# Kernel optimization log

Measured on AMD Instinct MI355X. Metric: run time of the kernel, lower is better.

Reference implementation:

```python
import jax, jax.numpy as jnp
import numpy as np

B, N, C, NH, AG, HW = 16, 3136, 256, 8, 49, 56

def setup_inputs() -> dict:
    key = jax.random.key(0)
    ks = jax.random.split(key, 14)
    f = lambda k, shp, s=0.02: jax.random.normal(k, shp, jnp.float32) * s
    return {
        "x_f": jax.random.normal(ks[0], (B, N, C), jnp.float32),
        "x_t": jax.random.normal(ks[1], (B, N, C), jnp.float32),
        "Wq": f(ks[2], (C, C)),
        "Wkv": f(ks[3], (C, 2 * C)),
        "Wproj": f(ks[4], (C, C)),
        "bproj": jnp.zeros((C,), jnp.float32),
        "dwc_w": f(ks[5], (C, 1, 3, 3), 0.1),   # depthwise 3x3, groups=C (OIHW, I=1)
        "dwc_b": jnp.zeros((C,), jnp.float32),
        "an_bias": f(ks[6], (NH, AG, 7, 7)),
        "na_bias": f(ks[7], (NH, AG, 7, 7)),
        "ah_bias": f(ks[8], (1, NH, AG, HW, 1)),
        "aw_bias": f(ks[9], (1, NH, AG, 1, HW)),
        "ha_bias": f(ks[10], (1, NH, HW, 1, AG)),
        "wa_bias": f(ks[11], (1, NH, 1, HW, AG)),
        "H": HW,
        "W": HW,
    }

def reference(x_f, x_t, Wq, Wkv, Wproj, bproj, dwc_w, dwc_b,
              an_bias, na_bias, ah_bias, aw_bias, ha_bias, wa_bias, H, W):
    b, n, c = x_f.shape
    h, ag = an_bias.shape[0], an_bias.shape[1]
    d = c // h
    scale = d ** (-0.5)
    ps = int(ag ** 0.5)  # agent grid side (7)

    q = x_f @ Wq                       # [b,n,c]
    kv = x_t @ Wkv                     # [b,n,2c]
    k, v = kv[..., :c], kv[..., c:]

    # agent tokens: adaptive avg-pool q over (H,W) -> (ps,ps); H%ps==0 so exact 8x8 block means
    agent = q.reshape(b, ps, H // ps, ps, W // ps, c).mean(axis=(2, 4)).reshape(b, ag, c)

    heads = lambda t, L: t.reshape(b, L, h, d).transpose(0, 2, 1, 3)
    qh, kh, vh, ah = heads(q, n), heads(k, n), heads(v, n), heads(agent, ag)

    # stage 1: agent <- kv attention, bias = bilinear(an_bias 7x7 -> HxW) + (ah + aw)
    pb1 = jax.image.resize(an_bias, (h, ag, H, W), method='bilinear').reshape(1, h, ag, n)
    pb2 = (ah_bias + aw_bias).reshape(1, h, ag, n)
    agent_attn = jax.nn.softmax(scale * jnp.einsum('bhad,bhnd->bhan', ah, kh) + pb1 + pb2, axis=-1)
    agent_v = jnp.einsum('bhan,bhnd->bhad', agent_attn, vh)  # [b,h,ag,d]

    # stage 2: query <- agent attention, bias = bilinear(na_bias)^T + (ha + wa)
    ab1 = jax.image.resize(na_bias, (h, ag, H, W), method='bilinear').reshape(1, h, ag, n).transpose(0, 1, 3, 2)
    ab2 = (ha_bias + wa_bias).reshape(1, h, n, ag)
    q_attn = jax.nn.softmax(scale * jnp.einsum('bhnd,bhad->bhna', qh, ah) + ab1 + ab2, axis=-1)
    x = jnp.einsum('bhna,bhad->bhnd', q_attn, agent_v).transpose(0, 2, 1, 3).reshape(b, n, c)

    # depthwise-conv residual on v
    v_img = vh.transpose(0, 2, 1, 3).reshape(b, H, W, c).transpose(0, 3, 1, 2)  # [b,c,H,W]
    dwc = jax.lax.conv_general_dilated(v_img, dwc_w, (1, 1), 'SAME',
                                       feature_group_count=c,
                                       dimension_numbers=('NCHW', 'OIHW', 'NCHW'))
    dwc = dwc + dwc_b[None, :, None, None]
    x = x + dwc.transpose(0, 2, 3, 1).reshape(b, n, c)

    return x @ Wproj + bproj
```

## Files before the change

### kernel.cpp

```cpp
#include <hip/hip_runtime.h>
#include <hip/hip_bf16.h>

namespace {
constexpr int kB  = 16;
constexpr int kN  = 3136;
constexpr int kC  = 256;
constexpr int kH  = 8;
constexpr int kD  = 32;
constexpr int kAG = 49;
constexpr int kHW = 56;
constexpr int kKV = 512;
constexpr int kSEG = 7;
constexpr int kPART = 33;

constexpr int BM = 128, BN = 128, BK = 64;
constexpr int LDK = BK + 8;

constexpr int kNT = kN / 256 + 1;
}

typedef __attribute__((ext_vector_type(8))) short short8;
typedef __attribute__((ext_vector_type(8))) unsigned short ushort8;
typedef __attribute__((ext_vector_type(4))) unsigned short ushort4v;
typedef __attribute__((ext_vector_type(4))) float f32x4;

__device__ __forceinline__ unsigned short f2bf(float f) {
  union { float f; unsigned u; } v; v.f = f;
  unsigned r = (v.u + 0x7FFF + ((v.u >> 16) & 1)) >> 16;
  return (unsigned short)r;
}
__device__ __forceinline__ float bf2f(unsigned short u) {
  union { unsigned u; float f; } v; v.u = ((unsigned)u) << 16;
  return v.f;
}

__device__ __forceinline__ float bilin7(const float* __restrict__ tab, int y, int x) {
  float fy = (y + 0.5f) * 0.125f - 0.5f;
  float fx = (x + 0.5f) * 0.125f - 0.5f;
  float fy0 = floorf(fy), fx0 = floorf(fx);
  float wy = fy - fy0, wx = fx - fx0;
  int y0 = (int)fy0, x0 = (int)fx0;
  int y0c = min(6, max(0, y0)),     x0c = min(6, max(0, x0));
  int y1c = min(6, max(0, y0 + 1)), x1c = min(6, max(0, x0 + 1));
  float v00 = tab[y0c * 7 + x0c], v01 = tab[y0c * 7 + x1c];
  float v10 = tab[y1c * 7 + x0c], v11 = tab[y1c * 7 + x1c];
  float top = v00 + wx * (v01 - v00);
  float bot = v10 + wx * (v11 - v10);
  return top + wy * (bot - top);
}

__global__ __launch_bounds__(256) void wtrans_kernel(
    const float* __restrict__ W, unsigned short* __restrict__ Wt, int K, int N) {
  int idx = blockIdx.x * 256 + threadIdx.x;
  if (idx >= K * N) return;
  int n = idx / K, k = idx - n * K;
  Wt[idx] = f2bf(W[(size_t)k * N + n]);
}

template <int AMODE, int OMODE>
__global__ __launch_bounds__(256) void gemm_mixed_kernel(
    const void* __restrict__ Ap, const unsigned short* __restrict__ Bt,
    const float* __restrict__ bias, void* __restrict__ Cp, void* __restrict__ Cp2,
    int M, int Nn, int K) {
  __shared__ unsigned short As[BM * LDK];
  __shared__ unsigned short Bs[BN * LDK];
  const int t = threadIdx.x;

  int tx = blockIdx.x, ty = blockIdx.y;
  {
    int nwg = gridDim.x * gridDim.y;
    if ((nwg & 7) == 0) {
      int bid = ty * gridDim.x + tx;
      int per8 = nwg >> 3;
      int lt = (bid & 7) * per8 + (bid >> 3);
      tx = lt % gridDim.x;
      ty = lt / gridDim.x;
    }
  }
  const int row0 = ty * BM;
  const int col0 = tx * BN;
  const int lane = t & 63;
  const int wid  = t >> 6;
  const int wrow = (wid >> 1) * 64;
  const int wcol = (wid & 1) * 64;
  const int lr = lane & 15, lg = lane >> 4;

  f32x4 acc[4][4] = {};

  for (int k0 = 0; k0 < K; k0 += BK) {
    __syncthreads();
    if constexpr (AMODE == 1) {
      const unsigned short* A = (const unsigned short*)Ap;
#pragma unroll
      for (int i = 0; i < 4; ++i) {
        int idx = t + i * 256;
        int r = idx >> 3, k8 = (idx & 7) * 8;
        int row = row0 + r;
        int bb = row / kN, nn = row - bb * kN;
        int k = k0 + k8;
        *(ushort8*)&As[r * LDK + k8] = *(const ushort8*)&A[
            (((size_t)bb * kH + (k >> 5)) * kN + nn) * kD + (k & 31)];
      }
    } else {
      const float* A = (const float*)Ap;
#pragma unroll
      for (int i = 0; i < 8; ++i) {
        int idx = t + i * 256;
        int r = idx >> 4, k4 = (idx & 15) * 4;
        float4 f = *(const float4*)&A[(size_t)(row0 + r) * K + k0 + k4];
        unsigned lo = (unsigned)f2bf(f.x) | ((unsigned)f2bf(f.y) << 16);
        unsigned hi = (unsigned)f2bf(f.z) | ((unsigned)f2bf(f.w) << 16);
        *(uint2*)&As[r * LDK + k4] = make_uint2(lo, hi);
      }
    }
#pragma unroll
    for (int i = 0; i < 4; ++i) {
      int idx = t + i * 256;
      int r = idx >> 3, k8 = (idx & 7) * 8;
      *(ushort8*)&Bs[r * LDK + k8] =
          *(const ushort8*)&Bt[(size_t)(col0 + r) * K + k0 + k8];
    }
    __syncthreads();
#pragma unroll
    for (int ks = 0; ks < 2; ++ks) {
      short8 af[4], bf[4];
#pragma unroll
      for (int m = 0; m < 4; ++m)
        af[m] = *(const short8*)&As[(wrow + m * 16 + lr) * LDK + ks * 32 + lg * 8];
#pragma unroll
      for (int n = 0; n < 4; ++n)
        bf[n] = *(const short8*)&Bs[(wcol + n * 16 + lr) * LDK + ks * 32 + lg * 8];
#pragma unroll
      for (int m = 0; m < 4; ++m)
#pragma unroll
        for (int n = 0; n < 4; ++n)
          acc[m][n] = __builtin_amdgcn_mfma_f32_16x16x32_bf16(
              af[m], bf[n], acc[m][n], 0, 0, 0);
    }
  }
#pragma unroll
  for (int m = 0; m < 4; ++m) {
#pragma unroll
    for (int n = 0; n < 4; ++n) {
      int col = col0 + wcol + n * 16 + lr;
      float badd = 0.f;
      if constexpr (OMODE == 0) badd = bias ? bias[col] : 0.f;
#pragma unroll
      for (int j = 0; j < 4; ++j) {
        int row = row0 + wrow + m * 16 + lg * 4 + j;
        if constexpr (OMODE == 0) {
          ((float*)Cp)[(size_t)row * Nn + col] = acc[m][n][j] + badd;
        } else {
          int bb = row / kN, nn = row - bb * kN;
          unsigned short val = f2bf(acc[m][n][j]);
          if constexpr (OMODE == 1) {
            ((unsigned short*)Cp)[(((size_t)bb * kH + (col >> 5)) * kN + nn) * kD
                                  + (col & 31)] = val;
          } else {
            if (col < kC)
              ((unsigned short*)Cp)[(((size_t)bb * kH + (col >> 5)) * kN + nn) * kD
                                    + (col & 31)] = val;
            else {
              int c2 = col - kC;
              ((unsigned short*)Cp2)[(((size_t)bb * kH + (c2 >> 5)) * kN + nn) * kD
                                     + (c2 & 31)] = val;
            }
          }
        }
      }
    }
  }
}

__global__ __launch_bounds__(256) void pool_kernel(const unsigned short* __restrict__ qT,
                                                   float* __restrict__ agent) {
  int blk = blockIdx.x;
  int b = blk / kAG, a = blk % kAG;
  int ho = a / 7, wo = a % 7;
  int c = threadIdx.x;
  int h = c >> 5, d = c & 31;
  const unsigned short* base = qT + ((size_t)b * kH + h) * kN * kD + d;
  float s = 0.f;
#pragma unroll
  for (int i = 0; i < 8; ++i) {
    int y = ho * 8 + i;
#pragma unroll
    for (int j = 0; j < 8; ++j) {
      int x = wo * 8 + j;
      s += bf2f(base[(size_t)(y * kHW + x) * kD]);
    }
  }
  agent[((size_t)b * kAG + a) * kC + c] = s * (1.f / 64.f);
}

__global__ __launch_bounds__(256) void abias_kernel(
    const float* __restrict__ an_bias, const float* __restrict__ ah_bias,
    const float* __restrict__ aw_bias, float* __restrict__ abias) {
  int ha = blockIdx.x;
  const float* tab = an_bias + ha * 49;
  const float* ahb = ah_bias + ha * kHW;
  const float* awb = aw_bias + ha * kHW;
  for (int n = threadIdx.x; n < kN; n += 256) {
    int y = n / kHW, x = n % kHW;
    abias[(size_t)ha * kN + n] = bilin7(tab, y, x) + ahb[y] + awb[x];
  }
}

__global__ __launch_bounds__(256) void agent_attn_flash4_kernel(
    const float* __restrict__ agent, const unsigned short* __restrict__ kT,
    const unsigned short* __restrict__ vT, const float* __restrict__ abias,
    float* __restrict__ part) {
  const int t = threadIdx.x;
  const int lin = blockIdx.x;
  const int h = lin & 7;
  const int r = lin >> 3;
  const int seg = r % kSEG;
  const int b = r / kSEG;
  const int w = t >> 6, lane = t & 63;
  const int lr = lane & 15, lg = lane >> 4;
  const float scale = 0.17677669529663687f;

  __shared__ char sh[36864];
  unsigned short* agsT = (unsigned short*)sh;
  unsigned short* Pa   = (unsigned short*)(sh + 5120) + w * 64 * 40;
  unsigned short* Vt   = (unsigned short*)(sh + 25600) + w * 32 * 40;
  float* lred = (float*)(sh + 35840);

  const unsigned short* kH_ = kT + ((size_t)b * kH + h) * kN * kD;
  const unsigned short* vH_ = vT + ((size_t)b * kH + h) * kN * kD;

  for (int i = t; i < 320; i += 256) *(ushort8*)&agsT[i * 8] = (ushort8)0;
  __syncthreads();
  for (int i = t; i < kAG * 4; i += 256) {
    int a = i >> 2, j = i & 3;
    const float* sp = agent + ((size_t)b * kAG + a) * kC + h * kD + j * 8;
    float4 f0 = *(const float4*)sp, f1 = *(const float4*)(sp + 4);
    ushort8 v;
    v[0] = f2bf(f0.x); v[1] = f2bf(f0.y); v[2] = f2bf(f0.z); v[3] = f2bf(f0.w);
    v[4] = f2bf(f1.x); v[5] = f2bf(f1.y); v[6] = f2bf(f1.z); v[7] = f2bf(f1.w);
    *(ushort8*)&agsT[a * 40 + j * 8] = v;
  }
  __syncthreads();

  float ls[4] = {};
  f32x4 o[4][2] = {};
  const int nchunks = (w < 2) ? 4 : 3;
  for (int ci = 0; ci < nchunks; ++ci) {
    const int chunk = w + 4 * ci;
    const int nb0 = seg * 448 + chunk * 32;
    {
      int n = lane & 31, d0 = (lane >> 5) * 16;
      const unsigned short* vp = vH_ + (size_t)(nb0 + n) * kD + d0;
      ushort8 v0 = *(const ushort8*)vp;
      ushort8 v1 = *(const ushort8*)(vp + 8);
#pragma unroll
      for (int e = 0; e < 8; ++e) Vt[(d0 + e) * 40 + n] = v0[e];
#pragma unroll
      for (int e = 0; e < 8; ++e) Vt[(d0 + 8 + e) * 40 + n] = v1[e];
    }
    short8 af0 = *(const short8*)&kH_[(size_t)(nb0 + lr) * kD + lg * 8];
    short8 af1 = *(const short8*)&kH_[(size_t)(nb0 + 16 + lr) * kD + lg * 8];
    f32x4 c[2][4] = {};
#pragma unroll
    for (int ct = 0; ct < 4; ++ct) {
      short8 bfr = *(const short8*)&agsT[(ct * 16 + lr) * 40 + lg * 8];
      c[0][ct] = __builtin_amdgcn_mfma_f32_16x16x32_bf16(af0, bfr, c[0][ct], 0, 0, 0);
      c[1][ct] = __builtin_amdgcn_mfma_f32_16x16x32_bf16(af1, bfr, c[1][ct], 0, 0, 0);
    }
#pragma unroll
    for (int rt = 0; rt < 2; ++rt) {
#pragma unroll
      for (int ct = 0; ct < 4; ++ct) {
        int a = ct * 16 + lr;
        bool valid = a < kAG;
        float4 ab = {0.f, 0.f, 0.f, 0.f};
        if (valid)
          ab = *(const float4*)&abias[((size_t)(h * kAG + a)) * kN + nb0 + rt * 16 + lg * 4];
        unsigned lo, hi;
        {
          float p0 = valid ? __expf(fmaf(c[rt][ct][0], scale, ab.x)) : 0.f;
          float p1 = valid ? __expf(fmaf(c[rt][ct][1], scale, ab.y)) : 0.f;
          float p2 = valid ? __expf(fmaf(c[rt][ct][2], scale, ab.z)) : 0.f;
          float p3 = valid ? __expf(fmaf(c[rt][ct][3], scale, ab.w)) : 0.f;
          ls[ct] += (p0 + p1) + (p2 + p3);
          lo = (unsigned)f2bf(p0) | ((unsigned)f2bf(p1) << 16);
          hi = (unsigned)f2bf(p2) | ((unsigned)f2bf(p3) << 16);
        }
        *(uint2*)&Pa[a * 40 + rt * 16 + lg * 4] = make_uint2(lo, hi);
      }
    }
    short8 bfv0 = *(const short8*)&Vt[(lr) * 40 + lg * 8];
    short8 bfv1 = *(const short8*)&Vt[(16 + lr) * 40 + lg * 8];
#pragma unroll
    for (int rt = 0; rt < 4; ++rt) {
      short8 afp = *(const short8*)&Pa[(rt * 16 + lr) * 40 + lg * 8];
      o[rt][0] = __builtin_amdgcn_mfma_f32_16x16x32_bf16(afp, bfv0, o[rt][0], 0, 0, 0);
      o[rt][1] = __builtin_amdgcn_mfma_f32_16x16x32_bf16(afp, bfv1, o[rt][1], 0, 0, 0);
    }
  }
#pragma unroll
  for (int ct = 0; ct < 4; ++ct) {
    ls[ct] += __shfl_xor(ls[ct], 16);
    ls[ct] += __shfl_xor(ls[ct], 32);
  }
  __syncthreads();
  float* ored = (float*)sh;
  if (lane < 16) {
#pragma unroll
    for (int ct = 0; ct < 4; ++ct) lred[w * 64 + ct * 16 + lane] = ls[ct];
  }
#pragma unroll
  for (int rt = 0; rt < 4; ++rt)
#pragma unroll
    for (int ct2 = 0; ct2 < 2; ++ct2)
#pragma unroll
      for (int reg = 0; reg < 4; ++reg)
        ored[(w * 64 + rt * 16 + lg * 4 + reg) * 33 + ct2 * 16 + lr] =
            o[rt][ct2][reg];
  __syncthreads();
  float* pb = part + (((size_t)(b * kH + h)) * kSEG + seg) * (kAG * kPART);
  if (t < kAG)
    pb[t * kPART] = lred[t] + lred[64 + t] + lred[128 + t] + lred[192 + t];
  for (int i = t; i < kAG * kD; i += 256) {
    int a = i >> 5, d = i & 31;
    float s = ored[a * 33 + d] + ored[(64 + a) * 33 + d]
            + ored[(128 + a) * 33 + d] + ored[(192 + a) * 33 + d];
    pb[a * kPART + 1 + d] = s;
  }
}

__global__ __launch_bounds__(256) void agent_merge_kernel(
    const float* __restrict__ part, float* __restrict__ agent_v) {
  int g = blockIdx.x * 256 + threadIdx.x;
  int d = g & 31;
  int a = (g >> 5) % kAG;
  int bh = g / (kAG * kD);
  const float* pb = part + (((size_t)bh) * kSEG) * (kAG * kPART) + a * kPART;
  float den = 0.f, num = 0.f;
#pragma unroll
  for (int s = 0; s < kSEG; ++s) {
    const float* p = pb + s * kAG * kPART;
    den += p[0];
    num += p[1 + d];
  }
  agent_v[g] = num / den;
}

__global__ __launch_bounds__(256) void qbias_kernel(
    const float* __restrict__ na_bias, const float* __restrict__ ha_bias,
    const float* __restrict__ wa_bias, unsigned short* __restrict__ qbias) {
  int ha = blockIdx.x;
  int h = ha / kAG, a = ha % kAG;
  const float* tab = na_bias + ha * 49;
  for (int n = threadIdx.x; n < kN; n += 256) {
    int y = n / kHW, x = n % kHW;
    qbias[(size_t)ha * kN + n] = f2bf(bilin7(tab, y, x)
        + ha_bias[(h * kHW + y) * kAG + a]
        + wa_bias[(h * kHW + x) * kAG + a]);
  }
}

__global__ __launch_bounds__(256) void qattn_v10_kernel(
    unsigned short* __restrict__ qT, const unsigned short* __restrict__ vT,
    const float* __restrict__ agent, const float* __restrict__ agent_v,
    const unsigned short* __restrict__ qbias, const float* __restrict__ dwc_w,
    const float* __restrict__ dwc_b) {
  const int t = threadIdx.x;
  int lin = blockIdx.x + gridDim.x * (blockIdx.y + gridDim.y * blockIdx.z);
  const int h = lin & 7;
  int rest = lin >> 3;
  const int n0 = (rest % kNT) * 256;
  const int b  = rest / kNT;
  const int w = t >> 6, lane = t & 63;
  const int lr = lane & 15, lg = lane >> 4;
  const float scale = 0.17677669529663687f;

  unsigned short* qH_ = qT + ((size_t)b * kH + h) * kN * kD;
  const unsigned short* vH_ = vT + ((size_t)b * kH + h) * kN * kD;

  __shared__ unsigned short agsT[64 * 40];
  __shared__ unsigned short avsT[32 * 72];
  __shared__ unsigned short PW[4][2560];

  for (int i = t; i < 320; i += 256) *(ushort8*)&agsT[i * 8] = (ushort8)0;
  for (int i = t; i < 288; i += 256) *(ushort8*)&avsT[i * 8] = (ushort8)0;
  __syncthreads();
  for (int i = t; i < kAG * 4; i += 256) {
    int a = i >> 2, j = i & 3;
    const float* sp = agent + ((size_t)b * kAG + a) * kC + h * kD + j * 8;
    float4 f0 = *(const float4*)sp, f1 = *(const float4*)(sp + 4);
    ushort8 v;
    v[0] = f2bf(f0.x); v[1] = f2bf(f0.y); v[2] = f2bf(f0.z); v[3] = f2bf(f0.w);
    v[4] = f2bf(f1.x); v[5] = f2bf(f1.y); v[6] = f2bf(f1.z); v[7] = f2bf(f1.w);
    *(ushort8*)&agsT[a * 40 + j * 8] = v;
  }
  for (int i = t; i < kAG * 8; i += 256) {
    int a = i >> 3, dj = i & 7;
    float4 f = *(const float4*)(agent_v + (((size_t)b * kH + h) * kAG + a) * kD + dj * 4);
    avsT[(dj * 4 + 0) * 72 + a] = f2bf(f.x);
    avsT[(dj * 4 + 1) * 72 + a] = f2bf(f.y);
    avsT[(dj * 4 + 2) * 72 + a] = f2bf(f.z);
    avsT[(dj * 4 + 3) * 72 + a] = f2bf(f.w);
  }
  __syncthreads();

  short8 af[4];
#pragma unroll
  for (int rt = 0; rt < 4; ++rt) {
    int nr = n0 + w * 64 + rt * 16 + lr;
    nr = min(nr, kN - 1);
    af[rt] = *(const short8*)&qH_[(size_t)nr * kD + lg * 8];
  }
  short8 bfr[4];
#pragma unroll
  for (int ct = 0; ct < 4; ++ct)
    bfr[ct] = *(const short8*)&agsT[(ct * 16 + lr) * 40 + lg * 8];
  f32x4 c[4][4] = {};
#pragma unroll
  for (int rt = 0; rt < 4; ++rt)
#pragma unroll
    for (int ct = 0; ct < 4; ++ct)
      c[rt][ct] = __builtin_amdgcn_mfma_f32_16x16x32_bf16(af[rt], bfr[ct],
                                                          c[rt][ct], 0, 0, 0);
  f32x4 lsumv[4] = {};
#pragma unroll
  for (int rt = 0; rt < 4; ++rt) {
#pragma unroll
    for (int ct = 0; ct < 4; ++ct) {
      int col = ct * 16 + lr;
      bool valid = col < kAG;
      int nrow = n0 + w * 64 + rt * 16 + lg * 4;
      nrow = min(nrow, kN - 4);
      float qb[4] = {0.f, 0.f, 0.f, 0.f};
      if (valid) {
        uint2 qw = *(const uint2*)&qbias[((size_t)(h * kAG + col)) * kN + nrow];
        qb[0] = bf2f((unsigned short)(qw.x & 0xffff));
        qb[1] = bf2f((unsigned short)(qw.x >> 16));
        qb[2] = bf2f((unsigned short)(qw.y & 0xffff));
        qb[3] = bf2f((unsigned short)(qw.y >> 16));
      }
#pragma unroll
      for (int reg = 0; reg < 4; ++reg) {
        float pv = valid ? __expf(fmaf(c[rt][ct][reg], scale, qb[reg])) : 0.f;
        c[rt][ct][reg] = pv;
        lsumv[rt][reg] += pv;
      }
    }
  }
#pragma unroll
  for (int rt = 0; rt < 4; ++rt)
#pragma unroll
    for (int j = 0; j < 4; ++j) {
      float v = lsumv[rt][j];
      v += __shfl_xor(v, 1);
      v += __shfl_xor(v, 2);
      v += __shfl_xor(v, 4);
      v += __shfl_xor(v, 8);
      lsumv[rt][j] = v;
    }
  unsigned short* Pw = PW[w];
  short8 bf2v[2][2];
#pragma unroll
  for (int ct2 = 0; ct2 < 2; ++ct2)
#pragma unroll
    for (int ks = 0; ks < 2; ++ks)
      bf2v[ct2][ks] = *(const short8*)&avsT[(ct2 * 16 + lr) * 72 + ks * 32 + lg * 8];
  f32x4 o[4][2] = {};
#pragma unroll
  for (int half = 0; half < 2; ++half) {
#pragma unroll
    for (int rt2 = 0; rt2 < 2; ++rt2)
#pragma unroll
      for (int ct = 0; ct < 4; ++ct)
#pragma unroll
        for (int reg = 0; reg < 4; ++reg)
          Pw[(rt2 * 16 + lg * 4 + reg) * 72 + ct * 16 + lr] =
              f2bf(c[half * 2 + rt2][ct][reg]);
#pragma unroll
    for (int rt2 = 0; rt2 < 2; ++rt2) {
      short8 afp[2];
#pragma unroll
      for (int ks = 0; ks < 2; ++ks)
        afp[ks] = *(const short8*)&Pw[(rt2 * 16 + lr) * 72 + ks * 32 + lg * 8];
      int rt = half * 2 + rt2;
#pragma unroll
      for (int ct2 = 0; ct2 < 2; ++ct2)
#pragma unroll
        for (int ks = 0; ks < 2; ++ks)
          o[rt][ct2] = __builtin_amdgcn_mfma_f32_16x16x32_bf16(
              afp[ks], bf2v[ct2][ks], o[rt][ct2], 0, 0, 0);
    }
  }
#pragma unroll
  for (int rt = 0; rt < 4; ++rt) {
    f32x4 inv;
#pragma unroll
    for (int j = 0; j < 4; ++j) inv[j] = 1.f / lsumv[rt][j];
#pragma unroll
    for (int ct2 = 0; ct2 < 2; ++ct2)
#pragma unroll
      for (int reg = 0; reg < 4; ++reg)
        Pw[(rt * 16 + lg * 4 + reg) * 36 + ct2 * 16 + lr] =
            f2bf(o[rt][ct2][reg] * inv[reg]);
  }
  const int n = n0 + t;
  if (n >= kN) return;
  const unsigned short* orow = &PW[w][(t & 63) * 36];
  float out[kD];
#pragma unroll
  for (int d4 = 0; d4 < 8; ++d4) {
    ushort4v v = *(const ushort4v*)&orow[d4 * 4];
#pragma unroll
    for (int e = 0; e < 4; ++e) out[d4 * 4 + e] = bf2f(v[e]);
  }
  const float* wb = dwc_w + (h * kD) * 9;
  const float* bb = dwc_b + h * kD;
#pragma unroll
  for (int d = 0; d < kD; ++d) out[d] += bb[d];
  const int y = n / kHW, x = n % kHW;
#pragma unroll
  for (int ky = 0; ky < 3; ++ky) {
    int yy = y + ky - 1;
    if (yy < 0 || yy >= kHW) continue;
#pragma unroll
    for (int kx = 0; kx < 3; ++kx) {
      int xx = x + kx - 1;
      if (xx < 0 || xx >= kHW) continue;
      const unsigned short* vp = vH_ + (size_t)(yy * kHW + xx) * kD;
#pragma unroll
      for (int d8 = 0; d8 < 4; ++d8) {
        ushort8 vv = *(const ushort8*)(vp + d8 * 8);
#pragma unroll
        for (int e = 0; e < 8; ++e)
          out[d8 * 8 + e] = fmaf(wb[(d8 * 8 + e) * 9 + ky * 3 + kx],
                                 bf2f(vv[e]), out[d8 * 8 + e]);
      }
    }
  }
  unsigned short* qp = qH_ + (size_t)n * kD;
#pragma unroll
  for (int d8 = 0; d8 < 4; ++d8) {
    ushort8 v;
#pragma unroll
    for (int e = 0; e < 8; ++e) v[e] = f2bf(out[d8 * 8 + e]);
    *(ushort8*)(qp + d8 * 8) = v;
  }
}

extern "C" void kernel_launch(void* const* d_in, const int* in_sizes, int n_in,
                              void* d_out, int out_size, void* d_ws, size_t ws_size,
                              hipStream_t stream) {
  const float* x_f     = (const float*)d_in[0];
  const float* x_t     = (const float*)d_in[1];
  const float* Wq      = (const float*)d_in[2];
  const float* Wkv     = (const float*)d_in[3];
  const float* Wproj   = (const float*)d_in[4];
  const float* bproj   = (const float*)d_in[5];
  const float* dwc_w   = (const float*)d_in[6];
  const float* dwc_b   = (const float*)d_in[7];
  const float* an_bias = (const float*)d_in[8];
  const float* na_bias = (const float*)d_in[9];
  const float* ah_bias = (const float*)d_in[10];
  const float* aw_bias = (const float*)d_in[11];
  const float* ha_bias = (const float*)d_in[12];
  const float* wa_bias = (const float*)d_in[13];
  float* out           = (float*)d_out;

  const size_t qbiasN = (size_t)kH * kAG * kN;
  const size_t wtE = (size_t)kC * kC + (size_t)kC * kKV + (size_t)kC * kC;
  const size_t tabB = qbiasN * 2 + qbiasN * 4 + wtE * 2;
  if (ws_size < tabB) return;

  const size_t headE = (size_t)kB * kH * kN * kD;
  const size_t qFullB   = headE * 2;
  const size_t agentB   = (size_t)kB * kAG * kC * 4;
  const size_t agentvB  = (size_t)kB * kH * kAG * kD * 4;
  const size_t partB    = (size_t)kB * kH * kSEG * kAG * kPART * 4;
  const size_t fullWsB  = tabB + qFullB + agentB + agentvB + partB;

  char* p = (char*)d_ws;
  unsigned short* qbias = (unsigned short*)p;  p += qbiasN * 2;
  float* abias = (float*)p;                    p += qbiasN * 4;
  unsigned short* WqT   = (unsigned short*)p;  p += (size_t)kC * kC * 2;
  unsigned short* WkvT  = (unsigned short*)p;  p += (size_t)kC * kKV * 2;
  unsigned short* WprojT= (unsigned short*)p;  p += (size_t)kC * kC * 2;

  qbias_kernel<<<kH * kAG, 256, 0, stream>>>(na_bias, ha_bias, wa_bias, qbias);
  abias_kernel<<<kH * kAG, 256, 0, stream>>>(an_bias, ah_bias, aw_bias, abias);
  wtrans_kernel<<<(kC * kC + 255) / 256, 256, 0, stream>>>(Wq, WqT, kC, kC);
  wtrans_kernel<<<(kC * kKV + 255) / 256, 256, 0, stream>>>(Wkv, WkvT, kC, kKV);
  wtrans_kernel<<<(kC * kC + 255) / 256, 256, 0, stream>>>(Wproj, WprojT, kC, kC);

  if (ws_size >= fullWsB) {
    unsigned short* qT = (unsigned short*)p;   p += qFullB;
    float* agent  = (float*)p;                 p += agentB;
    float* agentv = (float*)p;                 p += agentvB;
    float* part   = (float*)p;
    unsigned short* kT = (unsigned short*)d_out;
    unsigned short* vT = kT + headE;

    const int M = kB * kN;
    gemm_mixed_kernel<0, 1><<<dim3(kC / BN, M / BM), 256, 0, stream>>>(
        x_f, WqT, nullptr, qT, nullptr, M, kC, kC);
    gemm_mixed_kernel<0, 2><<<dim3(kKV / BN, M / BM), 256, 0, stream>>>(
        x_t, WkvT, nullptr, kT, vT, M, kKV, kC);
    pool_kernel<<<kB * kAG, 256, 0, stream>>>(qT, agent);
    agent_attn_flash4_kernel<<<kB * kH * kSEG, 256, 0, stream>>>(agent, kT, vT,
                                                                 abias, part);
    agent_merge_kernel<<<kB * kAG, 256, 0, stream>>>(part, agentv);
    qattn_v10_kernel<<<dim3(kNT, kH, kB), 256, 0, stream>>>(
        qT, vT, agent, agentv, qbias, dwc_w, dwc_b);
    gemm_mixed_kernel<1, 0><<<dim3(kC / BN, M / BM), 256, 0, stream>>>(
        qT, WprojT, bproj, out, nullptr, M, kC, kC);
    return;
  }

  const size_t perbB = (size_t)kH * kN * kD * 2 * 3
                     + ((size_t)kAG * kC + (size_t)kH * kAG * kD
                        + (size_t)kH * kSEG * kAG * kPART) * 4;
  size_t fit = (ws_size - tabB) / perbB;
  int chunk = (int)(fit < 16 ? fit : 16);
  if (chunk < 1) return;

  const size_t headEc = (size_t)chunk * kH * kN * kD;
  unsigned short* qT = (unsigned short*)p;     p += headEc * 2;
  unsigned short* kT = (unsigned short*)p;     p += headEc * 2;
  unsigned short* vT = (unsigned short*)p;     p += headEc * 2;
  float* agent  = (float*)p;                   p += (size_t)chunk * kAG * kC * 4;
  float* agentv = (float*)p;                   p += (size_t)chunk * kH * kAG * kD * 4;
  float* part   = (float*)p;

  for (int b0 = 0; b0 < kB; b0 += chunk) {
    int nb = (kB - b0) < chunk ? (kB - b0) : chunk;
    const int M = nb * kN;
    const float* xf_c = x_f + (size_t)b0 * kN * kC;
    const float* xt_c = x_t + (size_t)b0 * kN * kC;
    float* out_c = out + (size_t)b0 * kN * kC;

    gemm_mixed_kernel<0, 1><<<dim3(kC / BN, M / BM), 256, 0, stream>>>(
        xf_c, WqT, nullptr, qT, nullptr, M, kC, kC);
    gemm_mixed_kernel<0, 2><<<dim3(kKV / BN, M / BM), 256, 0, stream>>>(
        xt_c, WkvT, nullptr, kT, vT, M, kKV, kC);
    pool_kernel<<<nb * kAG, 256, 0, stream>>>(qT, agent);
    agent_attn_flash4_kernel<<<nb * kH * kSEG, 256, 0, stream>>>(agent, kT, vT,
                                                                 abias, part);
    agent_merge_kernel<<<nb * kAG, 256, 0, stream>>>(part, agentv);
    qattn_v10_kernel<<<dim3(kNT, kH, nb), 256, 0, stream>>>(
        qT, vT, agent, agentv, qbias, dwc_w, dwc_b);
    gemm_mixed_kernel<1, 0><<<dim3(kC / BN, M / BM), 256, 0, stream>>>(
        qT, WprojT, bproj, out_c, nullptr, M, kC, kC);
  }
}
```

Measured before the change: 190.7 us.

## Prefetch next K tile into registers during MFMA compute in GEMM

Restructures the GEMM main loop so global loads for the next K tile are issued into registers before the MFMA work on the current LDS tile, then written to LDS after a barrier. This is meant to hide global memory latency behind compute, in place of a load-sync-compute sequence. It raises register pressure (fp32 A staging uses 8 float4 per thread), which may lower occupancy.

```diff
diff --git a/kernel.cpp b/kernel.cpp
--- a/kernel.cpp
+++ b/kernel.cpp
@@ -85,10 +85,11 @@
   const int wcol = (wid & 1) * 64;
   const int lr = lane & 15, lg = lane >> 4;
 
-  f32x4 acc[4][4] = {};
-
-  for (int k0 = 0; k0 < K; k0 += BK) {
-    __syncthreads();
+  float4  aF[8];
+  ushort8 aB[4];
+  ushort8 bB[4];
+
+  auto loadA = [&](int k0) {
     if constexpr (AMODE == 1) {
       const unsigned short* A = (const unsigned short*)Ap;
 #pragma unroll
@@ -98,7 +99,7 @@
         int row = row0 + r;
         int bb = row / kN, nn = row - bb * kN;
         int k = k0 + k8;
-        *(ushort8*)&As[r * LDK + k8] = *(const ushort8*)&A[
+        aB[i] = *(const ushort8*)&A[
             (((size_t)bb * kH + (k >> 5)) * kN + nn) * kD + (k & 31)];
       }
     } else {
@@ -107,20 +108,53 @@
       for (int i = 0; i < 8; ++i) {
         int idx = t + i * 256;
         int r = idx >> 4, k4 = (idx & 15) * 4;
-        float4 f = *(const float4*)&A[(size_t)(row0 + r) * K + k0 + k4];
-        unsigned lo = (unsigned)f2bf(f.x) | ((unsigned)f2bf(f.y) << 16);
-        unsigned hi = (unsigned)f2bf(f.z) | ((unsigned)f2bf(f.w) << 16);
-        *(uint2*)&As[r * LDK + k4] = make_uint2(lo, hi);
-      }
-    }
+        aF[i] = *(const float4*)&A[(size_t)(row0 + r) * K + k0 + k4];
+      }
+    }
+  };
+  auto loadB = [&](int k0) {
 #pragma unroll
     for (int i = 0; i < 4; ++i) {
       int idx = t + i * 256;
       int r = idx >> 3, k8 = (idx & 7) * 8;
-      *(ushort8*)&Bs[r * LDK + k8] =
-          *(const ushort8*)&Bt[(size_t)(col0 + r) * K + k0 + k8];
-    }
-    __syncthreads();
+      bB[i] = *(const ushort8*)&Bt[(size_t)(col0 + r) * K + k0 + k8];
+    }
+  };
+  auto storeLDS = [&]() {
+    if constexpr (AMODE == 1) {
+#pragma unroll
+      for (int i = 0; i < 4; ++i) {
+        int idx = t + i * 256;
+        int r = idx >> 3, k8 = (idx & 7) * 8;
+        *(ushort8*)&As[r * LDK + k8] = aB[i];
+      }
+    } else {
+#pragma unroll
+      for (int i = 0; i < 8; ++i) {
+        int idx = t + i * 256;
+        int r = idx >> 4, k4 = (idx & 15) * 4;
+        unsigned lo = (unsigned)f2bf(aF[i].x) | ((unsigned)f2bf(aF[i].y) << 16);
+        unsigned hi = (unsigned)f2bf(aF[i].z) | ((unsigned)f2bf(aF[i].w) << 16);
+        *(uint2*)&As[r * LDK + k4] = make_uint2(lo, hi);
+      }
+    }
+#pragma unroll
+    for (int i = 0; i < 4; ++i) {
+      int idx = t + i * 256;
+      int r = idx >> 3, k8 = (idx & 7) * 8;
+      *(ushort8*)&Bs[r * LDK + k8] = bB[i];
+    }
+  };
+
+  f32x4 acc[4][4] = {};
+
+  loadA(0); loadB(0);
+  storeLDS();
+  __syncthreads();
+
+  for (int k0 = 0; k0 < K; k0 += BK) {
+    const bool more = (k0 + BK) < K;
+    if (more) { loadA(k0 + BK); loadB(k0 + BK); }
 #pragma unroll
     for (int ks = 0; ks < 2; ++ks) {
       short8 af[4], bf[4];
@@ -137,7 +171,13 @@
           acc[m][n] = __builtin_amdgcn_mfma_f32_16x16x32_bf16(
               af[m], bf[n], acc[m][n], 0, 0, 0);
     }
-  }
+    __syncthreads();
+    if (more) {
+      storeLDS();
+      __syncthreads();
+    }
+  }
+
 #pragma unroll
   for (int m = 0; m < 4; ++m) {
 #pragma unroll
```

After: 244.1 us. 1.28x slower.
